# Kernel optimization log

Hardware: AMD Instinct MI355X
Metric: run time of the kernel (lower is better)

Reference implementation:

```python
import jax, jax.numpy as jnp
import numpy as np

HOPS = 4
ALPHA = 0.1
N = 100000   # nodes
E = 1600000  # edges (before self loops)
DX = 128     # x feature dim
DY = 32      # y (soft label) dim


def setup_inputs() -> dict:
    key = jax.random.key(0)
    k1, k2, k3, k4 = jax.random.split(key, 4)
    x = jax.random.normal(k1, (N, DX), dtype=jnp.float32)
    y = jax.random.normal(k2, (N, DY), dtype=jnp.float32)
    src = jax.random.randint(k3, (E,), 0, N)
    dst = jax.random.randint(k4, (E,), 0, N)
    # emulate remove_self_loops with static shapes: perturb any accidental self loop
    dst = jnp.where(src == dst, (dst + 1) % N, dst)
    edge_index = jnp.stack([src, dst]).astype(jnp.int64)
    return {"x": x, "y": y, "edge_index": edge_index}


def reference(x, y, edge_index):
    src, dst = edge_index[0], edge_index[1]
    # add_self_loops (edge_index already has self loops removed)
    loop = jnp.arange(N, dtype=src.dtype)
    src = jnp.concatenate([src, loop])
    dst = jnp.concatenate([dst, loop])
    # symmetric normalization: w_e = deg(src)^-1/2 * deg(dst)^-1/2, deg counted on dst
    deg = jax.ops.segment_sum(jnp.ones_like(dst, dtype=x.dtype), dst, num_segments=N)
    dinv = jnp.where(deg > 0, deg ** -0.5, 0.0)
    w = dinv[src] * dinv[dst]  # [E+N]

    def spmm(v):
        # adj[src, dst] = w  =>  (adj @ v)[i] = sum_{e: src_e = i} w_e * v[dst_e]
        return jax.ops.segment_sum(w[:, None] * v[dst], src, num_segments=N)

    for _ in range(HOPS):
        x_prime = spmm(x)
        y_prime = spmm(y)
        if ALPHA > 0:
            x_prime = (1.0 - ALPHA) * x_prime + ALPHA * x
            y_prime = (1.0 - ALPHA) * y_prime + ALPHA * y
        x, y = x_prime, y_prime
    return x, y
```

## Files before the change

kernel.cpp:

```cpp
#include <hip/hip_runtime.h>
#include <hip/hip_fp16.h>


#define NN 100000
#define EE 1600000
#define NPAD 100096
#define NBKT 391
#define CHUNK 4096
#define CAP2 5120

#define GETREG_XCC_IMM (((32 - 1) << 11) | (0 << 6) | 20)

__device__ __forceinline__ unsigned packh(float a, float b) {
    __half2 h = __floats2half2_rn(a, b);
    return *reinterpret_cast<unsigned*>(&h);
}
__device__ __forceinline__ void acc8(float* a, uint4 w, float m) {
    const __half2* h = reinterpret_cast<const __half2*>(&w);
    #pragma unroll
    for (int i = 0; i < 4; ++i) {
        a[2 * i]     = fmaf(m, __half2float(__low2half(h[i])),  a[2 * i]);
        a[2 * i + 1] = fmaf(m, __half2float(__high2half(h[i])), a[2 * i + 1]);
    }
}
__device__ __forceinline__ void unp8(float* c, uint4 w) {
    const __half2* h = reinterpret_cast<const __half2*>(&w);
    #pragma unroll
    for (int i = 0; i < 4; ++i) {
        float2 f = __half22float2(h[i]);
        c[2 * i] = f.x; c[2 * i + 1] = f.y;
    }
}


__global__ void zero_kernel(int* __restrict__ bufs, int total,
                            const int* __restrict__ raw, int* __restrict__ flag) {
    int i = blockIdx.x * blockDim.x + threadIdx.x;
    if (i < total) bufs[i] = 0;
    if (i == 0) {
        int is64 = 1;
        for (int k = 1; k < 16; k += 2) {
            if (raw[k] != 0) { is64 = 0; break; }
        }
        *flag = is64;
    }
}

__global__ __launch_bounds__(256) void passA_kernel(const void* __restrict__ raw,
                                                    const int* __restrict__ flag,
                                                    int* __restrict__ indeg_rep,
                                                    int* __restrict__ gbcur,
                                                    int* __restrict__ buf) {
    __shared__ unsigned short sh_b[CHUNK];
    __shared__ unsigned int   sh_p[CHUNK];
    __shared__ unsigned int   sh_sorted[CHUNK];
    __shared__ unsigned short sh_bs[CHUNK];
    __shared__ int hist[512];
    __shared__ int excl[512];
    __shared__ int gbase[512];
    __shared__ int lcur[512];

    int tid = threadIdx.x;
    int base = blockIdx.x * CHUNK;
    int nval = EE - base; if (nval > CHUNK) nval = CHUNK;
    int r = __builtin_amdgcn_s_getreg(GETREG_XCC_IMM) & 7;
    int is64 = *flag;

    hist[tid] = 0; hist[tid + 256] = 0;
    __syncthreads();

    for (int i = tid; i < nval; i += 256) {
        int e = base + i;
        int s, d;
        if (is64) {
            s = (int)((const long long*)raw)[e];
            d = (int)((const long long*)raw)[EE + e];
        } else {
            s = ((const int*)raw)[e];
            d = ((const int*)raw)[EE + e];
        }
        atomicAdd(&indeg_rep[r * NPAD + d], 1);
        int b = s >> 8;
        sh_b[i] = (unsigned short)b;
        sh_p[i] = ((unsigned)(s & 255) << 17) | (unsigned)d;
        atomicAdd(&hist[b], 1);
    }
    __syncthreads();

    excl[tid] = hist[tid];
    excl[tid + 256] = hist[tid + 256];
    __syncthreads();
    for (int off = 1; off < 512; off <<= 1) {
        int a0 = (tid >= off) ? excl[tid - off] : 0;
        int a1 = (tid + 256 >= off) ? excl[tid + 256 - off] : 0;
        __syncthreads();
        excl[tid] += a0;
        excl[tid + 256] += a1;
        __syncthreads();
    }
    int inc0 = excl[tid], inc1 = excl[tid + 256];
    int h0 = hist[tid],  h1 = hist[tid + 256];
    __syncthreads();
    int e0 = inc0 - h0, e1 = inc1 - h1;
    excl[tid] = e0; excl[tid + 256] = e1;
    lcur[tid] = e0; lcur[tid + 256] = e1;
    if (h0 > 0) gbase[tid]       = atomicAdd(&gbcur[tid * 16], h0);
    if (h1 > 0) gbase[tid + 256] = atomicAdd(&gbcur[(tid + 256) * 16], h1);
    __syncthreads();

    for (int i = tid; i < nval; i += 256) {
        int b = sh_b[i];
        int pos = atomicAdd(&lcur[b], 1);
        sh_sorted[pos] = sh_p[i];
        sh_bs[pos] = (unsigned short)b;
    }
    __syncthreads();

    for (int i = tid; i < nval; i += 256) {
        int b = sh_bs[i];
        int gpos = gbase[b] + (i - excl[b]);
        if (gpos < CAP2)
            buf[(size_t)b * CAP2 + gpos] = (int)sh_sorted[i];
    }
}

__global__ void bucket_scan_kernel(const int* __restrict__ gbcur, int* __restrict__ bucket_base,
                                   int* __restrict__ rowptr) {
    __shared__ int s[512];
    int tid = threadIdx.x;
    int v = 0;
    if (tid < NBKT) {
        int c = gbcur[tid * 16];
        v = (c < CAP2) ? c : CAP2;
    }
    s[tid] = v;
    __syncthreads();
    for (int off = 1; off < 512; off <<= 1) {
        int t = (tid >= off) ? s[tid - off] : 0;
        __syncthreads();
        s[tid] += t;
        __syncthreads();
    }
    if (tid < NBKT) bucket_base[tid] = s[tid] - v;
    if (tid == 0) rowptr[NN] = EE;
}

__global__ void dinv_kernel(const int* __restrict__ indeg_rep, float* __restrict__ dinv) {
    int i = blockIdx.x * blockDim.x + threadIdx.x;
    if (i < NN) {
        int ind = 1;
        #pragma unroll
        for (int r = 0; r < 8; ++r) ind += indeg_rep[r * NPAD + i];
        dinv[i] = rsqrtf((float)ind);
    }
}

__global__ void cast_kernel(const float4* __restrict__ x0, const float4* __restrict__ y0,
                            const float* __restrict__ dinv, uint4* __restrict__ zx,
                            uint4* __restrict__ zy) {
    int t = blockIdx.x * blockDim.x + threadIdx.x;
    if (t < NN * 16) {
        int node = t >> 4, c = t & 15;
        float di = dinv[node];
        float4 a = x0[(size_t)node * 32 + c * 2];
        float4 b = x0[(size_t)node * 32 + c * 2 + 1];
        uint4 o;
        o.x = packh(di * a.x, di * a.y); o.y = packh(di * a.z, di * a.w);
        o.z = packh(di * b.x, di * b.y); o.w = packh(di * b.z, di * b.w);
        zx[(size_t)node * 16 + c] = o;
    } else if (t < NN * 20) {
        int u = t - NN * 16;
        int node = u >> 2, c = u & 3;
        float di = dinv[node];
        float4 a = y0[(size_t)node * 8 + c * 2];
        float4 b = y0[(size_t)node * 8 + c * 2 + 1];
        uint4 o;
        o.x = packh(di * a.x, di * a.y); o.y = packh(di * a.z, di * a.w);
        o.z = packh(di * b.x, di * b.y); o.w = packh(di * b.z, di * b.w);
        zy[(size_t)node * 4 + c] = o;
    }
}

__global__ __launch_bounds__(256) void passB_kernel(const int* __restrict__ gbcur,
                                                    const int* __restrict__ buf,
                                                    const int* __restrict__ bucket_base,
                                                    int* __restrict__ rowptr,
                                                    int* __restrict__ dst_sorted) {
    int b = blockIdx.x;
    int tid = threadIdx.x;
    __shared__ int edges[CAP2];
    __shared__ int hist[256];
    __shared__ int sc[256];
    __shared__ int base_s, tot_s;

    if (tid == 0) {
        int c = gbcur[b * 16];
        tot_s = (c < CAP2) ? c : CAP2;
        base_s = bucket_base[b];
    }
    hist[tid] = 0;
    __syncthreads();
    int total = tot_s;
    const int* src = buf + (size_t)b * CAP2;
    for (int i = tid; i < total; i += 256) {
        int p = src[i];
        edges[i] = p;
        atomicAdd(&hist[p >> 17], 1);
    }
    __syncthreads();
    int hv = hist[tid];
    sc[tid] = hv;
    __syncthreads();
    for (int o = 1; o < 256; o <<= 1) {
        int t = (tid >= o) ? sc[tid - o] : 0;
        __syncthreads();
        sc[tid] += t;
        __syncthreads();
    }
    int excl = sc[tid] - hv;
    int node = (b << 8) + tid;
    if (node < NN) rowptr[node] = base_s + excl;
    hist[tid] = excl;
    __syncthreads();
    for (int i = tid; i < total; i += 256) {
        int p = edges[i];
        int pos = atomicAdd(&hist[p >> 17], 1);
        dst_sorted[base_s + pos] = p & 0x1ffff;
    }
}

template <bool OUTH>
__global__ __launch_bounds__(256) void hop_kernel(const int* __restrict__ rowptr,
                                                  const int* __restrict__ dst_sorted,
                                                  const float* __restrict__ dinv,
                                                  const uint4* __restrict__ zx,
                                                  const uint4* __restrict__ zy,
                                                  void* __restrict__ nx,
                                                  void* __restrict__ ny) {
    int t = blockIdx.x * blockDim.x + threadIdx.x;
    int row = t >> 6, lane = t & 63;
    if (row >= NN) return;
    int beg = rowptr[row], end = rowptr[row + 1];
    float di = dinv[row];

    int g = lane >> 4, sub = lane & 15;
    int gy = lane >> 2, sy = lane & 3;

    float ax[8] = {0.f, 0.f, 0.f, 0.f, 0.f, 0.f, 0.f, 0.f};
    float ay[8] = {0.f, 0.f, 0.f, 0.f, 0.f, 0.f, 0.f, 0.f};

    int last = (end > beg) ? end - 1 : beg;
    for (int e0 = beg; e0 < end; e0 += 16) {
        int ex0 = e0 + g, ex1 = e0 + 4 + g, ex2 = e0 + 8 + g, ex3 = e0 + 12 + g;
        int ey = e0 + gy;
        int d0 = dst_sorted[min(ex0, last)];
        int d1 = dst_sorted[min(ex1, last)];
        int d2 = dst_sorted[min(ex2, last)];
        int d3 = dst_sorted[min(ex3, last)];
        int dy = dst_sorted[min(ey, last)];
        uint4 w0 = zx[(size_t)d0 * 16 + sub];
        uint4 w1 = zx[(size_t)d1 * 16 + sub];
        uint4 w2 = zx[(size_t)d2 * 16 + sub];
        uint4 w3 = zx[(size_t)d3 * 16 + sub];
        uint4 wy = zy[(size_t)dy * 4 + sy];
        float m0 = (ex0 <= last) ? 1.f : 0.f;
        float m1 = (ex1 <= last) ? 1.f : 0.f;
        float m2 = (ex2 <= last) ? 1.f : 0.f;
        float m3 = (ex3 <= last) ? 1.f : 0.f;
        float my = (ey  <= last) ? 1.f : 0.f;

        acc8(ax, w0, m0);
        acc8(ax, w1, m1);
        acc8(ax, w2, m2);
        acc8(ax, w3, m3);
        acc8(ay, wy, my);
    }

    #pragma unroll
    for (int m = 16; m <= 32; m <<= 1) {
        #pragma unroll
        for (int i = 0; i < 8; ++i) ax[i] += __shfl_xor(ax[i], m);
    }
    #pragma unroll
    for (int m = 4; m <= 32; m <<= 1) {
        #pragma unroll
        for (int i = 0; i < 8; ++i) ay[i] += __shfl_xor(ay[i], m);
    }

    float sg = 0.9f * di;
    float sl = 0.9f * di + 0.1f / di;

    if (g == 0) {
        uint4 wz = zx[(size_t)row * 16 + sub];
        float c[8];
        unp8(c, wz);
        float r[8];
        #pragma unroll
        for (int i = 0; i < 8; ++i) r[i] = sg * ax[i] + sl * c[i];
        if constexpr (OUTH) {
            uint4 o;
            o.x = packh(di * r[0], di * r[1]); o.y = packh(di * r[2], di * r[3]);
            o.z = packh(di * r[4], di * r[5]); o.w = packh(di * r[6], di * r[7]);
            ((uint4*)nx)[(size_t)row * 16 + sub] = o;
        } else {
            float4 a, b;
            a.x = r[0]; a.y = r[1]; a.z = r[2]; a.w = r[3];
            b.x = r[4]; b.y = r[5]; b.z = r[6]; b.w = r[7];
            ((float4*)nx)[(size_t)row * 32 + sub * 2]     = a;
            ((float4*)nx)[(size_t)row * 32 + sub * 2 + 1] = b;
        }
    }
    if (gy == 0) {
        uint4 wz = zy[(size_t)row * 4 + sy];
        float c[8];
        unp8(c, wz);
        float r[8];
        #pragma unroll
        for (int i = 0; i < 8; ++i) r[i] = sg * ay[i] + sl * c[i];
        if constexpr (OUTH) {
            uint4 o;
            o.x = packh(di * r[0], di * r[1]); o.y = packh(di * r[2], di * r[3]);
            o.z = packh(di * r[4], di * r[5]); o.w = packh(di * r[6], di * r[7]);
            ((uint4*)ny)[(size_t)row * 4 + sy] = o;
        } else {
            float4 a, b;
            a.x = r[0]; a.y = r[1]; a.z = r[2]; a.w = r[3];
            b.x = r[4]; b.y = r[5]; b.z = r[6]; b.w = r[7];
            ((float4*)ny)[(size_t)row * 8 + sy * 2]     = a;
            ((float4*)ny)[(size_t)row * 8 + sy * 2 + 1] = b;
        }
    }
}

extern "C" void kernel_launch(void* const* d_in, const int* in_sizes, int n_in,
                              void* d_out, int out_size, void* d_ws, size_t ws_size,
                              hipStream_t stream) {
    const float* x0  = (const float*)d_in[0];
    const float* y0  = (const float*)d_in[1];
    const void*  raw = d_in[2];

    float* out_x = (float*)d_out;
    float* out_y = out_x + (size_t)NN * 128;

    int*   flag        = (int*)d_ws;
    int*   indeg_rep   = flag + 16;
    int*   gbcur       = indeg_rep + 8 * NPAD;
    int*   bucket_base = gbcur + 512 * 16;
    int*   rowptr      = bucket_base + 512;
    float* dinv        = (float*)(rowptr + 100112);
    int*   buf         = (int*)(dinv + NPAD);
    int*   dst_sorted  = buf + (size_t)NBKT * CAP2;
    uint4* zxA         = (uint4*)(dst_sorted + EE);
    uint4* zxB         = zxA + (size_t)NN * 16;
    uint4* zyA         = (uint4*)(zxB + (size_t)NN * 16);
    uint4* zyB         = zyA + (size_t)NN * 4;

    const int B = 256;
    const int GW = (NN * 64 + B - 1) / B;
    const int ZTOT = 8 * NPAD + 512 * 16;

    zero_kernel<<<(ZTOT + B - 1) / B, B, 0, stream>>>(indeg_rep, ZTOT, (const int*)raw, flag);
    passA_kernel<<<(EE + CHUNK - 1) / CHUNK, 256, 0, stream>>>(raw, flag, indeg_rep, gbcur, buf);
    bucket_scan_kernel<<<1, 512, 0, stream>>>(gbcur, bucket_base, rowptr);
    dinv_kernel<<<(NN + B - 1) / B, B, 0, stream>>>(indeg_rep, dinv);
    cast_kernel<<<(NN * 20 + B - 1) / B, B, 0, stream>>>(
        (const float4*)x0, (const float4*)y0, dinv, zxA, zyA);
    passB_kernel<<<NBKT, 256, 0, stream>>>(gbcur, buf, bucket_base, rowptr, dst_sorted);

    hop_kernel<true><<<GW, B, 0, stream>>>(rowptr, dst_sorted, dinv, zxA, zyA, zxB, zyB);
    hop_kernel<true><<<GW, B, 0, stream>>>(rowptr, dst_sorted, dinv, zxB, zyB, zxA, zyA);
    hop_kernel<true><<<GW, B, 0, stream>>>(rowptr, dst_sorted, dinv, zxA, zyA, zxB, zyB);
    hop_kernel<false><<<GW, B, 0, stream>>>(rowptr, dst_sorted, dinv, zxB, zyB, out_x, out_y);
}
```

Before: 587.4 us.

## Split fused x/y hop kernel into separate x and y propagation kernels

```diff
diff --git a/kernel.cpp b/kernel.cpp
--- a/kernel.cpp
+++ b/kernel.cpp
@@ -230,13 +230,11 @@
 }
 
 template <bool OUTH>
-__global__ __launch_bounds__(256) void hop_kernel(const int* __restrict__ rowptr,
-                                                  const int* __restrict__ dst_sorted,
-                                                  const float* __restrict__ dinv,
-                                                  const uint4* __restrict__ zx,
-                                                  const uint4* __restrict__ zy,
-                                                  void* __restrict__ nx,
-                                                  void* __restrict__ ny) {
+__global__ __launch_bounds__(256) void hopx_kernel(const int* __restrict__ rowptr,
+                                                   const int* __restrict__ dst_sorted,
+                                                   const float* __restrict__ dinv,
+                                                   const uint4* __restrict__ zx,
+                                                   void* __restrict__ nx) {
     int t = blockIdx.x * blockDim.x + threadIdx.x;
     int row = t >> 6, lane = t & 63;
     if (row >= NN) return;
@@ -244,36 +242,27 @@
     float di = dinv[row];
 
     int g = lane >> 4, sub = lane & 15;
-    int gy = lane >> 2, sy = lane & 3;
 
     float ax[8] = {0.f, 0.f, 0.f, 0.f, 0.f, 0.f, 0.f, 0.f};
-    float ay[8] = {0.f, 0.f, 0.f, 0.f, 0.f, 0.f, 0.f, 0.f};
-
     int last = (end > beg) ? end - 1 : beg;
     for (int e0 = beg; e0 < end; e0 += 16) {
         int ex0 = e0 + g, ex1 = e0 + 4 + g, ex2 = e0 + 8 + g, ex3 = e0 + 12 + g;
-        int ey = e0 + gy;
         int d0 = dst_sorted[min(ex0, last)];
         int d1 = dst_sorted[min(ex1, last)];
         int d2 = dst_sorted[min(ex2, last)];
         int d3 = dst_sorted[min(ex3, last)];
-        int dy = dst_sorted[min(ey, last)];
         uint4 w0 = zx[(size_t)d0 * 16 + sub];
         uint4 w1 = zx[(size_t)d1 * 16 + sub];
         uint4 w2 = zx[(size_t)d2 * 16 + sub];
         uint4 w3 = zx[(size_t)d3 * 16 + sub];
-        uint4 wy = zy[(size_t)dy * 4 + sy];
         float m0 = (ex0 <= last) ? 1.f : 0.f;
         float m1 = (ex1 <= last) ? 1.f : 0.f;
         float m2 = (ex2 <= last) ? 1.f : 0.f;
         float m3 = (ex3 <= last) ? 1.f : 0.f;
-        float my = (ey  <= last) ? 1.f : 0.f;
-
         acc8(ax, w0, m0);
         acc8(ax, w1, m1);
         acc8(ax, w2, m2);
         acc8(ax, w3, m3);
-        acc8(ay, wy, my);
     }
 
     #pragma unroll
@@ -281,16 +270,10 @@
         #pragma unroll
         for (int i = 0; i < 8; ++i) ax[i] += __shfl_xor(ax[i], m);
     }
-    #pragma unroll
-    for (int m = 4; m <= 32; m <<= 1) {
-        #pragma unroll
-        for (int i = 0; i < 8; ++i) ay[i] += __shfl_xor(ay[i], m);
-    }
-
-    float sg = 0.9f * di;
-    float sl = 0.9f * di + 0.1f / di;
 
     if (g == 0) {
+        float sg = 0.9f * di;
+        float sl = 0.9f * di + 0.1f / di;
         uint4 wz = zx[(size_t)row * 16 + sub];
         float c[8];
         unp8(c, wz);
@@ -310,7 +293,45 @@
             ((float4*)nx)[(size_t)row * 32 + sub * 2 + 1] = b;
         }
     }
+}
+
+template <bool OUTH>
+__global__ __launch_bounds__(256) void hopy_kernel(const int* __restrict__ rowptr,
+                                                   const int* __restrict__ dst_sorted,
+                                                   const float* __restrict__ dinv,
+                                                   const uint4* __restrict__ zy,
+                                                   void* __restrict__ ny) {
+    int t = blockIdx.x * blockDim.x + threadIdx.x;
+    int row = t >> 6, lane = t & 63;
+    if (row >= NN) return;
+    int beg = rowptr[row], end = rowptr[row + 1];
+    float di = dinv[row];
+
+    int gy = lane >> 2, sy = lane & 3;
+
+    float ay[8] = {0.f, 0.f, 0.f, 0.f, 0.f, 0.f, 0.f, 0.f};
+    int last = (end > beg) ? end - 1 : beg;
+    for (int e0 = beg; e0 < end; e0 += 32) {
+        int e1 = e0 + gy, e2 = e0 + 16 + gy;
+        int d1 = dst_sorted[min(e1, last)];
+        int d2 = dst_sorted[min(e2, last)];
+        uint4 w1 = zy[(size_t)d1 * 4 + sy];
+        uint4 w2 = zy[(size_t)d2 * 4 + sy];
+        float m1 = (e1 <= last) ? 1.f : 0.f;
+        float m2 = (e2 <= last) ? 1.f : 0.f;
+        acc8(ay, w1, m1);
+        acc8(ay, w2, m2);
+    }
+
+    #pragma unroll
+    for (int m = 4; m <= 32; m <<= 1) {
+        #pragma unroll
+        for (int i = 0; i < 8; ++i) ay[i] += __shfl_xor(ay[i], m);
+    }
+
     if (gy == 0) {
+        float sg = 0.9f * di;
+        float sl = 0.9f * di + 0.1f / di;
         uint4 wz = zy[(size_t)row * 4 + sy];
         float c[8];
         unp8(c, wz);
@@ -367,8 +388,13 @@
         (const float4*)x0, (const float4*)y0, dinv, zxA, zyA);
     passB_kernel<<<NBKT, 256, 0, stream>>>(gbcur, buf, bucket_base, rowptr, dst_sorted);
 
-    hop_kernel<true><<<GW, B, 0, stream>>>(rowptr, dst_sorted, dinv, zxA, zyA, zxB, zyB);
-    hop_kernel<true><<<GW, B, 0, stream>>>(rowptr, dst_sorted, dinv, zxB, zyB, zxA, zyA);
-    hop_kernel<true><<<GW, B, 0, stream>>>(rowptr, dst_sorted, dinv, zxA, zyA, zxB, zyB);
-    hop_kernel<false><<<GW, B, 0, stream>>>(rowptr, dst_sorted, dinv, zxB, zyB, out_x, out_y);
-}
+    hopx_kernel<true><<<GW, B, 0, stream>>>(rowptr, dst_sorted, dinv, zxA, zxB);
+    hopx_kernel<true><<<GW, B, 0, stream>>>(rowptr, dst_sorted, dinv, zxB, zxA);
+    hopx_kernel<true><<<GW, B, 0, stream>>>(rowptr, dst_sorted, dinv, zxA, zxB);
+    hopx_kernel<false><<<GW, B, 0, stream>>>(rowptr, dst_sorted, dinv, zxB, out_x);
+
+    hopy_kernel<true><<<GW, B, 0, stream>>>(rowptr, dst_sorted, dinv, zyA, zyB);
+    hopy_kernel<true><<<GW, B, 0, stream>>>(rowptr, dst_sorted, dinv, zyB, zyA);
+    hopy_kernel<true><<<GW, B, 0, stream>>>(rowptr, dst_sorted, dinv, zyA, zyB);
+    hopy_kernel<false><<<GW, B, 0, stream>>>(rowptr, dst_sorted, dinv, zyB, out_y);
+}
```

New measurement: 600.1 us. +2.2%, slower.
